# Kernel tuning notes

Measured on AMD Instinct MI355X. Metric: run time of the kernel, lower is better.

The kernel has to match this reference:

```python
import jax, jax.numpy as jnp
import numpy as np

H = 1024
B = 8
T = 2048

def setup_inputs() -> dict:
    key = jax.random.key(0)
    ks = jax.random.split(key, 12)
    s = 1.0 / np.sqrt(H)
    return {
        "x": jax.random.normal(ks[0], (B, T, H), dtype=jnp.float32),
        "time_decay": jax.random.normal(ks[1], (H,), dtype=jnp.float32) * 0.1,
        "time_first": jax.random.normal(ks[2], (H,), dtype=jnp.float32) * 0.1,
        "time_mix_key": jax.random.uniform(ks[3], (1, 1, H), dtype=jnp.float32),
        "time_mix_value": jax.random.uniform(ks[4], (1, 1, H), dtype=jnp.float32),
        "time_mix_receptance": jax.random.uniform(ks[5], (1, 1, H), dtype=jnp.float32),
        "Wk": jax.random.normal(ks[6], (H, H), dtype=jnp.float32) * s,
        "Wv": jax.random.normal(ks[7], (H, H), dtype=jnp.float32) * s,
        "Wr": jax.random.normal(ks[8], (H, H), dtype=jnp.float32) * s,
        "Wo": jax.random.normal(ks[9], (H, H), dtype=jnp.float32) * s,
        "bo": jax.random.normal(ks[10], (H,), dtype=jnp.float32) * 0.01,
    }

def reference(x, time_decay, time_first, time_mix_key, time_mix_value,
              time_mix_receptance, Wk, Wv, Wr, Wo, bo):
    # time shift: shifted[:, t] = x[:, t-1], shifted[:, 0] = 0
    shifted = jnp.pad(x, ((0, 0), (1, 0), (0, 0)))[:, :-1]
    k_in = x * time_mix_key + shifted * (1.0 - time_mix_key)
    v_in = x * time_mix_value + shifted * (1.0 - time_mix_value)
    r_in = x * time_mix_receptance + shifted * (1.0 - time_mix_receptance)
    k = jnp.einsum('bth,oh->bto', k_in, Wk)
    v = jnp.einsum('bth,oh->bto', v_in, Wv)
    r = jax.nn.sigmoid(jnp.einsum('bth,oh->bto', r_in, Wr))

    td = jnp.exp(-jnp.exp(time_decay))  # (H,)

    def step(carry, kv):
        num, den = carry            # (B, H) each
        k_t, v_t = kv               # (B, H) each
        e = jnp.exp(time_first + k_t)
        out_t = (num + e * v_t) / (den + e)
        ek = jnp.exp(k_t)
        return (td * num + ek * v_t, td * den + ek), out_t

    init = (jnp.zeros((x.shape[0], x.shape[2]), x.dtype),
            jnp.zeros((x.shape[0], x.shape[2]), x.dtype))
    # scan over time: (T, B, H)
    _, wkv = jax.lax.scan(step, init, (k.transpose(1, 0, 2), v.transpose(1, 0, 2)))
    wkv = wkv.transpose(1, 0, 2)    # (B, T, H)

    return jnp.einsum('bth,oh->bto', r * wkv, Wo) + bo
```

## Files before the change

kernel.cpp:

```cpp
#include <hip/hip_runtime.h>
#include <hip/hip_bf16.h>
#include <cstdint>
#include <cstddef>

#define HH 1024
#define BB 8
#define TT 2048
#define MM (BB*TT)
#define CC 64
#define LL (TT/CC)

typedef __attribute__((ext_vector_type(8))) short bf16x8;
typedef __attribute__((ext_vector_type(16))) float f32x16;

__device__ __forceinline__ unsigned short f2bf(float f) {
  union { float f; unsigned u; } v; v.f = f;
  return (unsigned short)((v.u + 0x7fffu + ((v.u >> 16) & 1u)) >> 16);
}
__device__ __forceinline__ float bf2f(unsigned short s) {
  union { float f; unsigned u; } v; v.u = ((unsigned)s) << 16;
  return v.f;
}

__device__ __forceinline__ void load_lds16(const void* g, void* l) {
  __builtin_amdgcn_global_load_lds((const __attribute__((address_space(1))) void*)g,
                                   (__attribute__((address_space(3))) void*)l,
                                   16, 0, 0);
}

__global__ __launch_bounds__(256) void conv_w(const float* __restrict__ Wk,
    const float* __restrict__ Wv, const float* __restrict__ Wr,
    const float* __restrict__ Wo, unsigned short* __restrict__ dst) {
  const int i = (blockIdx.x * 256 + threadIdx.x) * 4;
  const float* src = blockIdx.y == 0 ? Wk : blockIdx.y == 1 ? Wv : blockIdx.y == 2 ? Wr : Wo;
  const float4 v = *(const float4*)(src + i);
  ushort4 o; o.x = f2bf(v.x); o.y = f2bf(v.y); o.z = f2bf(v.z); o.w = f2bf(v.w);
  *(ushort4*)(dst + (size_t)blockIdx.y * HH * HH + i) = o;
}

__global__ __launch_bounds__(256) void mix_kernel(const float* __restrict__ x,
    const float* __restrict__ tmk, const float* __restrict__ tmv, const float* __restrict__ tmr,
    unsigned short* __restrict__ kin, unsigned short* __restrict__ vin,
    unsigned short* __restrict__ rin) {
  const int gid = blockIdx.x * 256 + threadIdx.x;
  const size_t e0 = (size_t)gid * 4;
  const int h = (int)(e0 & (HH - 1));
  const int t = (int)((e0 >> 10) & (TT - 1));
  const float4 xv = *(const float4*)(x + e0);
  float4 sv = make_float4(0.f, 0.f, 0.f, 0.f);
  if (t != 0) sv = *(const float4*)(x + e0 - HH);
  const float4 k4 = *(const float4*)(tmk + h);
  const float4 v4 = *(const float4*)(tmv + h);
  const float4 r4 = *(const float4*)(tmr + h);
  ushort4 ko, vo, ro;
  ko.x = f2bf(sv.x + k4.x * (xv.x - sv.x)); ko.y = f2bf(sv.y + k4.y * (xv.y - sv.y));
  ko.z = f2bf(sv.z + k4.z * (xv.z - sv.z)); ko.w = f2bf(sv.w + k4.w * (xv.w - sv.w));
  vo.x = f2bf(sv.x + v4.x * (xv.x - sv.x)); vo.y = f2bf(sv.y + v4.y * (xv.y - sv.y));
  vo.z = f2bf(sv.z + v4.z * (xv.z - sv.z)); vo.w = f2bf(sv.w + v4.w * (xv.w - sv.w));
  ro.x = f2bf(sv.x + r4.x * (xv.x - sv.x)); ro.y = f2bf(sv.y + r4.y * (xv.y - sv.y));
  ro.z = f2bf(sv.z + r4.z * (xv.z - sv.z)); ro.w = f2bf(sv.w + r4.w * (xv.w - sv.w));
  *(ushort4*)(kin + e0) = ko;
  *(ushort4*)(vin + e0) = vo;
  *(ushort4*)(rin + e0) = ro;
}

__device__ __forceinline__ void gemm_core32(const unsigned short* __restrict__ Ag,
                                            const unsigned short* __restrict__ Bg,
                                            int m0, int n0,
                                            unsigned short* As, unsigned short* Bs,
                                            f32x16 acc[2][2]) {
  const int tid = threadIdx.x;
  const int lane = tid & 63;
  const int w = tid >> 6;
  const int K = HH;
  const int c0 = tid, c1 = 256 + tid;
  const int r0 = c0 >> 2, s0 = c0 & 3, q0 = s0 ^ ((r0 >> 1) & 3);
  const int r1 = c1 >> 2, s1 = c1 & 3, q1 = s1 ^ ((r1 >> 1) & 3);
  const unsigned short* ga0 = Ag + (size_t)(m0 + r0) * K + q0 * 8;
  const unsigned short* ga1 = Ag + (size_t)(m0 + r1) * K + q1 * 8;
  const unsigned short* gb0 = Bg + (size_t)(n0 + r0) * K + q0 * 8;
  const unsigned short* gb1 = Bg + (size_t)(n0 + r1) * K + q1 * 8;
  unsigned short* la0 = As + (size_t)w * 512;
  unsigned short* la1 = As + 2048 + (size_t)w * 512;
  unsigned short* lb0 = Bs + (size_t)w * 512;
  unsigned short* lb1 = Bs + 2048 + (size_t)w * 512;
  const int wm = w >> 1, wn = w & 1;
  const int l31 = lane & 31, lh = lane >> 5;
  const int arow0 = wm * 64 + l31;
  const int brow0 = wn * 64 + l31;

  for (int kt = 0; kt < K; kt += 32) {
    load_lds16(ga0 + kt, la0);
    load_lds16(ga1 + kt, la1);
    load_lds16(gb0 + kt, lb0);
    load_lds16(gb1 + kt, lb1);
    __syncthreads();
    bf16x8 af[2][2], bfr[2][2];
#pragma unroll
    for (int c = 0; c < 2; c++) {
      const int kq = c * 2 + lh;
#pragma unroll
      for (int mi = 0; mi < 2; mi++) {
        const int ar = arow0 + mi * 32;
        af[mi][c] = *(const bf16x8*)(As + ar * 32 + (kq ^ ((ar >> 1) & 3)) * 8);
      }
#pragma unroll
      for (int nj = 0; nj < 2; nj++) {
        const int br = brow0 + nj * 32;
        bfr[nj][c] = *(const bf16x8*)(Bs + br * 32 + (kq ^ ((br >> 1) & 3)) * 8);
      }
    }
#pragma unroll
    for (int c = 0; c < 2; c++)
#pragma unroll
      for (int mi = 0; mi < 2; mi++)
#pragma unroll
        for (int nj = 0; nj < 2; nj++)
          acc[mi][nj] = __builtin_amdgcn_mfma_f32_32x32x16_bf16(af[mi][c], bfr[nj][c],
                                                                acc[mi][nj], 0, 0, 0);
    __syncthreads();
  }
}

__device__ __forceinline__ void swizzle_mn(int x, int& m0, int& n0) {
  const int xcd = x & 7;
  const int t = x >> 3;
  const int bn = t & 7;
  const int bml = t >> 3;
  m0 = (xcd * 16 + bml) * 128;
  n0 = bn * 128;
}

__global__ __launch_bounds__(256) void gemm_kvr(const unsigned short* __restrict__ kin,
    const unsigned short* __restrict__ vin, const unsigned short* __restrict__ rin,
    const unsigned short* __restrict__ Wbf,
    unsigned short* __restrict__ kb, unsigned short* __restrict__ vb,
    unsigned short* __restrict__ rb) {
  __shared__ unsigned short As[128 * 32];
  __shared__ unsigned short Bs[128 * 32];
  const int z = blockIdx.y;
  const unsigned short* Ag = z == 0 ? kin : (z == 1 ? vin : rin);
  const unsigned short* Bg = Wbf + (size_t)z * HH * HH;
  unsigned short* Cg = z == 0 ? kb : (z == 1 ? vb : rb);
  int m0, n0; swizzle_mn(blockIdx.x, m0, n0);
  f32x16 acc[2][2] = {};
  gemm_core32(Ag, Bg, m0, n0, As, Bs, acc);
  const int lane = threadIdx.x & 63, w = threadIdx.x >> 6;
  const int wm = w >> 1, wn = w & 1, l31 = lane & 31, lh = lane >> 5;
  const bool sig = (z == 2);
#pragma unroll
  for (int mi = 0; mi < 2; mi++)
#pragma unroll
    for (int nj = 0; nj < 2; nj++) {
      const int col = n0 + wn * 64 + nj * 32 + l31;
      const int rb0 = m0 + wm * 64 + mi * 32 + 4 * lh;
#pragma unroll
      for (int reg = 0; reg < 16; reg++) {
        const int row = rb0 + (reg & 3) + 8 * (reg >> 2);
        float vv = acc[mi][nj][reg];
        if (sig) vv = 1.0f / (1.0f + __expf(-vv));
        Cg[(size_t)row * HH + col] = f2bf(vv);
      }
    }
}

__global__ __launch_bounds__(256) void gemm_o(const unsigned short* __restrict__ Ag,
    const unsigned short* __restrict__ Bg, const float* __restrict__ bias,
    float* __restrict__ C) {
  __shared__ unsigned short As[128 * 32];
  __shared__ unsigned short Bs[128 * 32];
  int m0, n0; swizzle_mn(blockIdx.x, m0, n0);
  f32x16 acc[2][2] = {};
  gemm_core32(Ag, Bg, m0, n0, As, Bs, acc);
  const int lane = threadIdx.x & 63, w = threadIdx.x >> 6;
  const int wm = w >> 1, wn = w & 1, l31 = lane & 31, lh = lane >> 5;
#pragma unroll
  for (int mi = 0; mi < 2; mi++)
#pragma unroll
    for (int nj = 0; nj < 2; nj++) {
      const int col = n0 + wn * 64 + nj * 32 + l31;
      const float bv = bias[col];
      const int rb0 = m0 + wm * 64 + mi * 32 + 4 * lh;
#pragma unroll
      for (int reg = 0; reg < 16; reg++) {
        const int row = rb0 + (reg & 3) + 8 * (reg >> 2);
        C[(size_t)row * HH + col] = acc[mi][nj][reg] + bv;
      }
    }
}

__global__ __launch_bounds__(256) void wkv_part(const unsigned short* __restrict__ k,
    const unsigned short* __restrict__ v, const float* __restrict__ tdec,
    float* __restrict__ pnum, float* __restrict__ pden) {
  const int gid = blockIdx.x * 256 + threadIdx.x;
  const int h = gid & (HH - 1);
  const int bh = gid & (BB * HH - 1);
  const int b = (gid >> 10) & (BB - 1);
  const int c = gid >> 13;
  const float td = __expf(-__expf(tdec[h]));
  size_t idx = (size_t)b * TT * HH + (size_t)(c * LL) * HH + h;
  float num = 0.f, den = 0.f;
#pragma unroll 8
  for (int i = 0; i < LL; ++i, idx += HH) {
    const float ek = __expf(bf2f(k[idx]));
    const float vt = bf2f(v[idx]);
    num = td * num + ek * vt;
    den = td * den + ek;
  }
  pnum[(size_t)c * (BB * HH) + bh] = num;
  pden[(size_t)c * (BB * HH) + bh] = den;
}

__global__ __launch_bounds__(256) void wkv_scan(const float* __restrict__ tdec,
    float* __restrict__ pnum, float* __restrict__ pden) {
  const int bh = blockIdx.x * 256 + threadIdx.x;
  const int h = bh & (HH - 1);
  const float ed = __expf(tdec[h]);
  const float tdL = __expf(-ed * (float)LL);
  float num = 0.f, den = 0.f;
#pragma unroll 8
  for (int c = 0; c < CC; ++c) {
    const size_t o = (size_t)c * (BB * HH) + bh;
    const float tn = pnum[o], td_ = pden[o];
    pnum[o] = num; pden[o] = den;
    num = tdL * num + tn;
    den = tdL * den + td_;
  }
}

__global__ __launch_bounds__(256) void wkv_final(const unsigned short* __restrict__ k,
    const unsigned short* __restrict__ v, const unsigned short* __restrict__ r,
    const float* __restrict__ tdec, const float* __restrict__ tfst,
    const float* __restrict__ pnum, const float* __restrict__ pden,
    unsigned short* __restrict__ rwkv) {
  const int gid = blockIdx.x * 256 + threadIdx.x;
  const int h = gid & (HH - 1);
  const int bh = gid & (BB * HH - 1);
  const int b = (gid >> 10) & (BB - 1);
  const int c = gid >> 13;
  const float td = __expf(-__expf(tdec[h]));
  const float etf = __expf(tfst[h]);
  float num = pnum[(size_t)c * (BB * HH) + bh];
  float den = pden[(size_t)c * (BB * HH) + bh];
  size_t idx = (size_t)b * TT * HH + (size_t)(c * LL) * HH + h;
#pragma unroll 4
  for (int i = 0; i < LL; ++i, idx += HH) {
    const float ek = __expf(bf2f(k[idx]));
    const float vt = bf2f(v[idx]);
    const float rt = bf2f(r[idx]);
    const float e = ek * etf;
    const float inv = __builtin_amdgcn_rcpf(den + e);
    const float outv = (num + e * vt) * inv;
    num = td * num + ek * vt;
    den = td * den + ek;
    rwkv[idx] = f2bf(outv * rt);
  }
}

extern "C" void kernel_launch(void* const* d_in, const int* in_sizes, int n_in,
                              void* d_out, int out_size, void* d_ws, size_t ws_size,
                              hipStream_t stream) {
  (void)in_sizes; (void)n_in; (void)out_size; (void)ws_size;
  const float* x    = (const float*)d_in[0];
  const float* tdec = (const float*)d_in[1];
  const float* tfst = (const float*)d_in[2];
  const float* tmk  = (const float*)d_in[3];
  const float* tmv  = (const float*)d_in[4];
  const float* tmr  = (const float*)d_in[5];
  const float* Wk   = (const float*)d_in[6];
  const float* Wv   = (const float*)d_in[7];
  const float* Wr   = (const float*)d_in[8];
  const float* Wo   = (const float*)d_in[9];
  const float* bo   = (const float*)d_in[10];
  float* out = (float*)d_out;

  char* ws = (char*)d_ws;
  const size_t MiB = (size_t)1 << 20;
  unsigned short* Wbf = (unsigned short*)(ws);
  unsigned short* kin = (unsigned short*)(ws + 8 * MiB);
  unsigned short* vin = (unsigned short*)(ws + 40 * MiB);
  unsigned short* rin = (unsigned short*)(ws + 72 * MiB);
  unsigned short* rb  = (unsigned short*)(ws + 104 * MiB);
  unsigned short* kb = (unsigned short*)out;
  unsigned short* vb = kb + (size_t)MM * HH;
  unsigned short* rwkv = kin;
  float* pnum = (float*)(ws + 40 * MiB);
  float* pden = (float*)(ws + 42 * MiB);

  hipLaunchKernelGGL(conv_w, dim3(1024, 4), dim3(256), 0, stream, Wk, Wv, Wr, Wo, Wbf);
  hipLaunchKernelGGL(mix_kernel, dim3(16384), dim3(256), 0, stream,
                     x, tmk, tmv, tmr, kin, vin, rin);
  hipLaunchKernelGGL(gemm_kvr, dim3(1024, 3), dim3(256), 0, stream,
                     kin, vin, rin, Wbf, kb, vb, rb);
  hipLaunchKernelGGL(wkv_part, dim3(2048), dim3(256), 0, stream,
                     kb, vb, tdec, pnum, pden);
  hipLaunchKernelGGL(wkv_scan, dim3(32), dim3(256), 0, stream,
                     tdec, pnum, pden);
  hipLaunchKernelGGL(wkv_final, dim3(2048), dim3(256), 0, stream,
                     kb, vb, rb, tdec, tfst, pnum, pden, rwkv);
  hipLaunchKernelGGL(gemm_o, dim3(1024), dim3(256), 0, stream,
                     rwkv, Wbf + (size_t)3 * HH * HH, bo, out);
}
```

Baseline: 383.6 us.

## Merge weight-convert into mix kernel, fold chunk scan into final, use 16x16 MFMA

Weight conversion and the time-shift mix now run in one launch, with the block index choosing which job each block does. The separate chunk-prefix scan kernel is removed: each wkv_final thread recomputes its own prefix by looping over the earlier chunk states, which adds redundant reads and work for later chunks. Both GEMMs switch from 32x32x16 to 16x16x32 bf16 MFMA tiles with a 4x4 accumulator grid per wave. Together these cut two kernel launches and change the MFMA shape and fragment layout.

Result: slower. 410.0 us (+6.9%).

```diff
diff --git a/kernel.cpp b/kernel.cpp
--- a/kernel.cpp
+++ b/kernel.cpp
@@ -11,7 +11,7 @@
 #define LL (TT/CC)
 
 typedef __attribute__((ext_vector_type(8))) short bf16x8;
-typedef __attribute__((ext_vector_type(16))) float f32x16;
+typedef __attribute__((ext_vector_type(4))) float f32x4;
 
 __device__ __forceinline__ unsigned short f2bf(float f) {
   union { float f; unsigned u; } v; v.f = f;
@@ -28,21 +28,24 @@
                                    16, 0, 0);
 }
 
-__global__ __launch_bounds__(256) void conv_w(const float* __restrict__ Wk,
-    const float* __restrict__ Wv, const float* __restrict__ Wr,
-    const float* __restrict__ Wo, unsigned short* __restrict__ dst) {
-  const int i = (blockIdx.x * 256 + threadIdx.x) * 4;
-  const float* src = blockIdx.y == 0 ? Wk : blockIdx.y == 1 ? Wv : blockIdx.y == 2 ? Wr : Wo;
-  const float4 v = *(const float4*)(src + i);
-  ushort4 o; o.x = f2bf(v.x); o.y = f2bf(v.y); o.z = f2bf(v.z); o.w = f2bf(v.w);
-  *(ushort4*)(dst + (size_t)blockIdx.y * HH * HH + i) = o;
-}
-
-__global__ __launch_bounds__(256) void mix_kernel(const float* __restrict__ x,
+__global__ __launch_bounds__(256) void prep_kernel(const float* __restrict__ x,
     const float* __restrict__ tmk, const float* __restrict__ tmv, const float* __restrict__ tmr,
+    const float* __restrict__ Wk, const float* __restrict__ Wv,
+    const float* __restrict__ Wr, const float* __restrict__ Wo,
     unsigned short* __restrict__ kin, unsigned short* __restrict__ vin,
-    unsigned short* __restrict__ rin) {
-  const int gid = blockIdx.x * 256 + threadIdx.x;
+    unsigned short* __restrict__ rin, unsigned short* __restrict__ Wbf) {
+  const int bx = blockIdx.x;
+  if (bx >= 16384) {
+    const int bl = bx - 16384;
+    const int wsel = bl >> 10;
+    const int i = ((bl & 1023) * 256 + threadIdx.x) * 4;
+    const float* src = wsel == 0 ? Wk : wsel == 1 ? Wv : wsel == 2 ? Wr : Wo;
+    const float4 v = *(const float4*)(src + i);
+    ushort4 o; o.x = f2bf(v.x); o.y = f2bf(v.y); o.z = f2bf(v.z); o.w = f2bf(v.w);
+    *(ushort4*)(Wbf + (size_t)wsel * HH * HH + i) = o;
+    return;
+  }
+  const int gid = bx * 256 + threadIdx.x;
   const size_t e0 = (size_t)gid * 4;
   const int h = (int)(e0 & (HH - 1));
   const int t = (int)((e0 >> 10) & (TT - 1));
@@ -64,18 +67,18 @@
   *(ushort4*)(rin + e0) = ro;
 }
 
-__device__ __forceinline__ void gemm_core32(const unsigned short* __restrict__ Ag,
-                                            const unsigned short* __restrict__ Bg,
-                                            int m0, int n0,
-                                            unsigned short* As, unsigned short* Bs,
-                                            f32x16 acc[2][2]) {
+__device__ __forceinline__ void gemm_core(const unsigned short* __restrict__ Ag,
+                                          const unsigned short* __restrict__ Bg,
+                                          int m0, int n0,
+                                          unsigned short* As, unsigned short* Bs,
+                                          f32x4 acc[4][4]) {
   const int tid = threadIdx.x;
   const int lane = tid & 63;
   const int w = tid >> 6;
   const int K = HH;
   const int c0 = tid, c1 = 256 + tid;
-  const int r0 = c0 >> 2, s0 = c0 & 3, q0 = s0 ^ ((r0 >> 1) & 3);
-  const int r1 = c1 >> 2, s1 = c1 & 3, q1 = s1 ^ ((r1 >> 1) & 3);
+  const int r0 = c0 >> 2, q0 = (c0 & 3) ^ ((r0 >> 1) & 3);
+  const int r1 = c1 >> 2, q1 = (c1 & 3) ^ ((r1 >> 1) & 3);
   const unsigned short* ga0 = Ag + (size_t)(m0 + r0) * K + q0 * 8;
   const unsigned short* ga1 = Ag + (size_t)(m0 + r1) * K + q1 * 8;
   const unsigned short* gb0 = Bg + (size_t)(n0 + r0) * K + q0 * 8;
@@ -85,9 +88,7 @@
   unsigned short* lb0 = Bs + (size_t)w * 512;
   unsigned short* lb1 = Bs + 2048 + (size_t)w * 512;
   const int wm = w >> 1, wn = w & 1;
-  const int l31 = lane & 31, lh = lane >> 5;
-  const int arow0 = wm * 64 + l31;
-  const int brow0 = wn * 64 + l31;
+  const int fr = lane & 15, fq = lane >> 4;
 
   for (int kt = 0; kt < K; kt += 32) {
     load_lds16(ga0 + kt, la0);
@@ -95,29 +96,22 @@
     load_lds16(gb0 + kt, lb0);
     load_lds16(gb1 + kt, lb1);
     __syncthreads();
-    bf16x8 af[2][2], bfr[2][2];
-#pragma unroll
-    for (int c = 0; c < 2; c++) {
-      const int kq = c * 2 + lh;
-#pragma unroll
-      for (int mi = 0; mi < 2; mi++) {
-        const int ar = arow0 + mi * 32;
-        af[mi][c] = *(const bf16x8*)(As + ar * 32 + (kq ^ ((ar >> 1) & 3)) * 8);
-      }
-#pragma unroll
-      for (int nj = 0; nj < 2; nj++) {
-        const int br = brow0 + nj * 32;
-        bfr[nj][c] = *(const bf16x8*)(Bs + br * 32 + (kq ^ ((br >> 1) & 3)) * 8);
-      }
+    bf16x8 af[4], bfr[4];
+#pragma unroll
+    for (int i = 0; i < 4; i++) {
+      const int ar = wm * 64 + i * 16 + fr;
+      af[i] = *(const bf16x8*)(As + ar * 32 + ((fq ^ ((ar >> 1) & 3)) * 8));
     }
 #pragma unroll
-    for (int c = 0; c < 2; c++)
-#pragma unroll
-      for (int mi = 0; mi < 2; mi++)
-#pragma unroll
-        for (int nj = 0; nj < 2; nj++)
-          acc[mi][nj] = __builtin_amdgcn_mfma_f32_32x32x16_bf16(af[mi][c], bfr[nj][c],
-                                                                acc[mi][nj], 0, 0, 0);
+    for (int j = 0; j < 4; j++) {
+      const int br = wn * 64 + j * 16 + fr;
+      bfr[j] = *(const bf16x8*)(Bs + br * 32 + ((fq ^ ((br >> 1) & 3)) * 8));
+    }
+#pragma unroll
+    for (int i = 0; i < 4; i++)
+#pragma unroll
+      for (int j = 0; j < 4; j++)
+        acc[i][j] = __builtin_amdgcn_mfma_f32_16x16x32_bf16(af[i], bfr[j], acc[i][j], 0, 0, 0);
     __syncthreads();
   }
 }
@@ -143,25 +137,23 @@
   const unsigned short* Bg = Wbf + (size_t)z * HH * HH;
   unsigned short* Cg = z == 0 ? kb : (z == 1 ? vb : rb);
   int m0, n0; swizzle_mn(blockIdx.x, m0, n0);
-  f32x16 acc[2][2] = {};
-  gemm_core32(Ag, Bg, m0, n0, As, Bs, acc);
+  f32x4 acc[4][4] = {};
+  gemm_core(Ag, Bg, m0, n0, As, Bs, acc);
   const int lane = threadIdx.x & 63, w = threadIdx.x >> 6;
-  const int wm = w >> 1, wn = w & 1, l31 = lane & 31, lh = lane >> 5;
+  const int wm = w >> 1, wn = w & 1, fr = lane & 15, fq = lane >> 4;
   const bool sig = (z == 2);
 #pragma unroll
-  for (int mi = 0; mi < 2; mi++)
-#pragma unroll
-    for (int nj = 0; nj < 2; nj++) {
-      const int col = n0 + wn * 64 + nj * 32 + l31;
-      const int rb0 = m0 + wm * 64 + mi * 32 + 4 * lh;
-#pragma unroll
-      for (int reg = 0; reg < 16; reg++) {
-        const int row = rb0 + (reg & 3) + 8 * (reg >> 2);
-        float vv = acc[mi][nj][reg];
+  for (int i = 0; i < 4; i++)
+#pragma unroll
+    for (int j = 0; j < 4; j++)
+#pragma unroll
+      for (int rr = 0; rr < 4; rr++) {
+        const int row = m0 + wm * 64 + i * 16 + fq * 4 + rr;
+        const int col = n0 + wn * 64 + j * 16 + fr;
+        float vv = acc[i][j][rr];
         if (sig) vv = 1.0f / (1.0f + __expf(-vv));
         Cg[(size_t)row * HH + col] = f2bf(vv);
       }
-    }
 }
 
 __global__ __launch_bounds__(256) void gemm_o(const unsigned short* __restrict__ Ag,
@@ -170,21 +162,20 @@
   __shared__ unsigned short As[128 * 32];
   __shared__ unsigned short Bs[128 * 32];
   int m0, n0; swizzle_mn(blockIdx.x, m0, n0);
-  f32x16 acc[2][2] = {};
-  gemm_core32(Ag, Bg, m0, n0, As, Bs, acc);
+  f32x4 acc[4][4] = {};
+  gemm_core(Ag, Bg, m0, n0, As, Bs, acc);
   const int lane = threadIdx.x & 63, w = threadIdx.x >> 6;
-  const int wm = w >> 1, wn = w & 1, l31 = lane & 31, lh = lane >> 5;
-#pragma unroll
-  for (int mi = 0; mi < 2; mi++)
-#pragma unroll
-    for (int nj = 0; nj < 2; nj++) {
-      const int col = n0 + wn * 64 + nj * 32 + l31;
+  const int wm = w >> 1, wn = w & 1, fr = lane & 15, fq = lane >> 4;
+#pragma unroll
+  for (int i = 0; i < 4; i++)
+#pragma unroll
+    for (int j = 0; j < 4; j++) {
+      const int col = n0 + wn * 64 + j * 16 + fr;
       const float bv = bias[col];
-      const int rb0 = m0 + wm * 64 + mi * 32 + 4 * lh;
-#pragma unroll
-      for (int reg = 0; reg < 16; reg++) {
-        const int row = rb0 + (reg & 3) + 8 * (reg >> 2);
-        C[(size_t)row * HH + col] = acc[mi][nj][reg] + bv;
+#pragma unroll
+      for (int rr = 0; rr < 4; rr++) {
+        const int row = m0 + wm * 64 + i * 16 + fq * 4 + rr;
+        C[(size_t)row * HH + col] = acc[i][j][rr] + bv;
       }
     }
 }
@@ -211,23 +202,6 @@
   pden[(size_t)c * (BB * HH) + bh] = den;
 }
 
-__global__ __launch_bounds__(256) void wkv_scan(const float* __restrict__ tdec,
-    float* __restrict__ pnum, float* __restrict__ pden) {
-  const int bh = blockIdx.x * 256 + threadIdx.x;
-  const int h = bh & (HH - 1);
-  const float ed = __expf(tdec[h]);
-  const float tdL = __expf(-ed * (float)LL);
-  float num = 0.f, den = 0.f;
-#pragma unroll 8
-  for (int c = 0; c < CC; ++c) {
-    const size_t o = (size_t)c * (BB * HH) + bh;
-    const float tn = pnum[o], td_ = pden[o];
-    pnum[o] = num; pden[o] = den;
-    num = tdL * num + tn;
-    den = tdL * den + td_;
-  }
-}
-
 __global__ __launch_bounds__(256) void wkv_final(const unsigned short* __restrict__ k,
     const unsigned short* __restrict__ v, const unsigned short* __restrict__ r,
     const float* __restrict__ tdec, const float* __restrict__ tfst,
@@ -238,10 +212,16 @@
   const int bh = gid & (BB * HH - 1);
   const int b = (gid >> 10) & (BB - 1);
   const int c = gid >> 13;
-  const float td = __expf(-__expf(tdec[h]));
+  const float ed = __expf(tdec[h]);
+  const float td = __expf(-ed);
+  const float tdL = __expf(-ed * (float)LL);
   const float etf = __expf(tfst[h]);
-  float num = pnum[(size_t)c * (BB * HH) + bh];
-  float den = pden[(size_t)c * (BB * HH) + bh];
+  float num = 0.f, den = 0.f;
+  for (int cc = 0; cc < c; ++cc) {
+    const size_t o = (size_t)cc * (BB * HH) + bh;
+    num = tdL * num + pnum[o];
+    den = tdL * den + pden[o];
+  }
   size_t idx = (size_t)b * TT * HH + (size_t)(c * LL) * HH + h;
 #pragma unroll 4
   for (int i = 0; i < LL; ++i, idx += HH) {
@@ -287,15 +267,12 @@
   float* pnum = (float*)(ws + 40 * MiB);
   float* pden = (float*)(ws + 42 * MiB);
 
-  hipLaunchKernelGGL(conv_w, dim3(1024, 4), dim3(256), 0, stream, Wk, Wv, Wr, Wo, Wbf);
-  hipLaunchKernelGGL(mix_kernel, dim3(16384), dim3(256), 0, stream,
-                     x, tmk, tmv, tmr, kin, vin, rin);
+  hipLaunchKernelGGL(prep_kernel, dim3(16384 + 4096), dim3(256), 0, stream,
+                     x, tmk, tmv, tmr, Wk, Wv, Wr, Wo, kin, vin, rin, Wbf);
   hipLaunchKernelGGL(gemm_kvr, dim3(1024, 3), dim3(256), 0, stream,
                      kin, vin, rin, Wbf, kb, vb, rb);
   hipLaunchKernelGGL(wkv_part, dim3(2048), dim3(256), 0, stream,
                      kb, vb, tdec, pnum, pden);
-  hipLaunchKernelGGL(wkv_scan, dim3(32), dim3(256), 0, stream,
-                     tdec, pnum, pden);
   hipLaunchKernelGGL(wkv_final, dim3(2048), dim3(256), 0, stream,
                      kb, vb, rb, tdec, tfst, pnum, pden, rwkv);
   hipLaunchKernelGGL(gemm_o, dim3(1024), dim3(256), 0, stream,
```
